# Optimization experiments

Measured on AMD Instinct MI355X. Metric: run time of the kernel, lower is better.

## Reference

```python
import jax, jax.numpy as jnp
import numpy as np

B = 1024      # molecules (segments)
K = 16        # conformers per molecule
N = B * K     # total nodes
C = 128       # in_out_dimension
HID = 256     # hidden_dimension of gate MLP
HEADS = 2
LAYERS = 2


def _leaky(x, slope):
    return jnp.where(x >= 0, x, slope * x)


def setup_inputs() -> dict:
    key = jax.random.key(0)
    ks = jax.random.split(key, 12)
    # segment ids: K conformers per molecule, sorted
    batch = jnp.repeat(jnp.arange(B, dtype=jnp.int64), K)
    # fully connected within each segment, no self loops, then append self loops
    idx = np.arange(N, dtype=np.int64).reshape(B, K)
    src = np.broadcast_to(idx[:, :, None], (B, K, K)).reshape(-1)
    dst = np.broadcast_to(idx[:, None, :], (B, K, K)).reshape(-1)
    keep = src != dst
    e_src = jnp.asarray(np.concatenate([src[keep], np.arange(N, dtype=np.int64)]))
    e_dst = jnp.asarray(np.concatenate([dst[keep], np.arange(N, dtype=np.int64)]))
    sc = 1.0 / np.sqrt(C)
    sh = 1.0 / np.sqrt(HID)
    inp = {
        "H": jax.random.normal(ks[0], (N, C), jnp.float32),
        "batch": batch,
        "edge_src": e_src,
        "edge_dst": e_dst,
        "Wl": jax.random.normal(ks[1], (LAYERS, C, HEADS * C), jnp.float32) * sc,
        "bl": jnp.zeros((LAYERS, HEADS * C), jnp.float32),
        "Wr": jax.random.normal(ks[2], (LAYERS, C, HEADS * C), jnp.float32) * sc,
        "br": jnp.zeros((LAYERS, HEADS * C), jnp.float32),
        "att": jax.random.normal(ks[3], (LAYERS, HEADS, C), jnp.float32) * sc,
        "gat_bias": jnp.zeros((LAYERS, C), jnp.float32),
        "gW1": jax.random.normal(ks[4], (C, HID), jnp.float32) * sc,
        "gb1": jnp.zeros((HID,), jnp.float32),
        "gW2": jax.random.normal(ks[5], (HID, HID), jnp.float32) * sh,
        "gb2": jnp.zeros((HID,), jnp.float32),
        "gW3": jax.random.normal(ks[6], (HID, 1), jnp.float32) * sh,
        "gb3": jnp.zeros((1,), jnp.float32),
    }
    return inp


def _segment_softmax(logits, seg, num_segments):
    m = jax.ops.segment_max(logits, seg, num_segments=num_segments)
    ex = jnp.exp(logits - m[seg])
    den = jax.ops.segment_sum(ex, seg, num_segments=num_segments)
    return ex / den[seg]


def _gatv2(x, e_src, e_dst, Wl, bl, Wr, br, att, bias):
    # GATv2Conv, concat=False (mean over heads), negative_slope=0.2
    xl = (x @ Wl + bl).reshape(N, HEADS, C)   # source transform
    xr = (x @ Wr + br).reshape(N, HEADS, C)   # target transform
    e = _leaky(xl[e_src] + xr[e_dst], 0.2)    # [E, H, C]
    logits = jnp.einsum('ehc,hc->eh', e, att) # [E, H]
    alpha = _segment_softmax(logits, e_dst, N)
    out = jax.ops.segment_sum(xl[e_src] * alpha[:, :, None], e_dst, num_segments=N)
    return out.mean(axis=1) + bias            # [N, C]


def reference(H, batch, edge_src, edge_dst, Wl, bl, Wr, br, att, gat_bias,
              gW1, gb1, gW2, gb2, gW3, gb3):
    x = H
    for l in range(LAYERS):
        x = _gatv2(x, edge_src, edge_dst, Wl[l], bl[l], Wr[l], br[l], att[l], gat_bias[l])
    # gate MLP (LeakyReLU default slope 0.01)
    h = _leaky(x @ gW1 + gb1, 0.01)
    h = _leaky(h @ gW2 + gb2, 0.01)
    h_gate = h @ gW3 + gb3                    # [N, 1]
    scores = _segment_softmax(h_gate, batch, B)
    h_pool = jax.ops.segment_sum(x * scores, batch, num_segments=B)  # [B, C]
    return (h_pool, scores)
```

## Files before the change

### kernel.cpp

```cpp
#include <hip/hip_runtime.h>
#include <hip/hip_bf16.h>
#include <math.h>

#define N_NODES 16384
#define B_MOL   1024

typedef __attribute__((ext_vector_type(8))) short short8v;
typedef __attribute__((ext_vector_type(4))) float f32x4;

static __device__ __forceinline__ unsigned short f2bf(float f) {
    unsigned int u = __float_as_uint(f);
    unsigned int r = (u + 0x7FFFu + ((u >> 16) & 1u)) >> 16;
    return (unsigned short)r;
}
static __device__ __forceinline__ float bf2f(unsigned short h) {
    return __uint_as_float(((unsigned int)h) << 16);
}

__global__ __launch_bounds__(256)
void conv_pack(const float* __restrict__ Wl, const float* __restrict__ Wr,
               const float* __restrict__ g1, const float* __restrict__ g2,
               unsigned short* __restrict__ wpk) {
    int idx = blockIdx.x * 256 + threadIdx.x;
    if (idx >= 229376) return;
    float v; size_t base; int nK, k, col;
    if (idx < 131072) {
        int l = idx >> 16;
        int e = idx & 65535;
        k = e >> 9; col = e & 511;
        v = (col < 256) ? Wl[l * 32768 + k * 256 + col]
                        : Wr[l * 32768 + k * 256 + (col - 256)];
        base = (size_t)l * 131072; nK = 4;
    } else if (idx < 163840) {
        int e = idx - 131072; k = e >> 8; col = e & 255;
        v = g1[k * 256 + col]; base = 262144; nK = 4;
    } else {
        int e = idx - 163840; k = e >> 8; col = e & 255;
        v = g2[k * 256 + col]; base = 327680; nK = 8;
    }
    int cb = col >> 4, ci = col & 15, ks = k >> 5, kk = k & 31;
    int lane = ((kk >> 3) << 4) | ci;
    size_t fo = ((size_t)(cb * nK + ks) * 2) * 512 + lane * 8 + (kk & 7);
    unsigned short h = f2bf(v);
    wpk[base + fo] = h;
    wpk[base + fo + 512] = f2bf(v - bf2f(h));
}

template<int NK, int NCB>
static __device__ __forceinline__ void tile_gemm32(
        const short* __restrict__ Ah, const short* __restrict__ Al,
        const unsigned short* __restrict__ wv,
        f32x4 (&acc)[2][NCB], int lane) {
    int lr = lane & 15;
    int kq = (lane >> 4) * 8;
    short8v bc[NCB][2], bn[NCB][2];
    #pragma unroll
    for (int j = 0; j < NCB; ++j) {
        bc[j][0] = *(const short8v*)&wv[((j * NK + 0) * 2 + 0) * 512 + lane * 8];
        bc[j][1] = *(const short8v*)&wv[((j * NK + 0) * 2 + 1) * 512 + lane * 8];
    }
    #pragma unroll
    for (int ks = 0; ks < NK; ++ks) {
        if (ks + 1 < NK) {
            #pragma unroll
            for (int j = 0; j < NCB; ++j) {
                bn[j][0] = *(const short8v*)&wv[((j * NK + ks + 1) * 2 + 0) * 512 + lane * 8];
                bn[j][1] = *(const short8v*)&wv[((j * NK + ks + 1) * 2 + 1) * 512 + lane * 8];
            }
        }
        short8v ah[2], al[2];
        #pragma unroll
        for (int i = 0; i < 2; ++i) {
            int ro = (i * 16 + lr) * 264 + ks * 32 + kq;
            ah[i] = *(const short8v*)&Ah[ro];
            al[i] = *(const short8v*)&Al[ro];
        }
        #pragma unroll
        for (int i = 0; i < 2; ++i)
            #pragma unroll
            for (int j = 0; j < NCB; ++j) {
                acc[i][j] = __builtin_amdgcn_mfma_f32_16x16x32_bf16(ah[i], bc[j][0], acc[i][j], 0, 0, 0);
                acc[i][j] = __builtin_amdgcn_mfma_f32_16x16x32_bf16(ah[i], bc[j][1], acc[i][j], 0, 0, 0);
                acc[i][j] = __builtin_amdgcn_mfma_f32_16x16x32_bf16(al[i], bc[j][0], acc[i][j], 0, 0, 0);
            }
        if (ks + 1 < NK) {
            #pragma unroll
            for (int j = 0; j < NCB; ++j) { bc[j][0] = bn[j][0]; bc[j][1] = bn[j][1]; }
        }
    }
}

static __device__ __forceinline__ void pack_pair(f32x4 o, short4* ph, short4* pl) {
    unsigned short h0 = f2bf(o[0]), h1 = f2bf(o[1]), h2 = f2bf(o[2]), h3 = f2bf(o[3]);
    *ph = make_short4((short)h0, (short)h1, (short)h2, (short)h3);
    *pl = make_short4((short)f2bf(o[0] - bf2f(h0)), (short)f2bf(o[1] - bf2f(h1)),
                      (short)f2bf(o[2] - bf2f(h2)), (short)f2bf(o[3] - bf2f(h3)));
}

__global__ __launch_bounds__(1024)
void mega(const float* __restrict__ H, const unsigned short* __restrict__ wpk,
          const float* __restrict__ bl, const float* __restrict__ br,
          const float* __restrict__ att, const float* __restrict__ gbias,
          const float* __restrict__ gb1, const float* __restrict__ gb2,
          const float* __restrict__ gW3, const float* __restrict__ gb3,
          float* __restrict__ out) {
    __shared__ short sAh[32][264], sAl[32][264];
    __shared__ float sL[32][260], sR[32][260];
    __shared__ float sLog[2][32][20];
    __shared__ float sAtt[512];
    __shared__ float sg[32], ssc[32];

    int tid  = threadIdx.x;
    int lane = tid & 63;
    int w    = tid >> 6;
    int lr   = lane & 15;
    int rowBase = blockIdx.x * 32;

    {
        int r = tid >> 5, q = tid & 31;
        f32x4 v = *(const f32x4*)&H[(size_t)(rowBase + r) * 128 + q * 4];
        pack_pair(v, (short4*)&sAh[r][q * 4], (short4*)&sAl[r][q * 4]);
        if (tid < 512) sAtt[tid] = att[tid];
    }
    __syncthreads();

    for (int l = 0; l < 2; ++l) {
        {
            #pragma unroll
            for (int p = 0; p < 2; ++p) {
                f32x4 acc[2][1];
                acc[0][0] = (f32x4){0.f, 0.f, 0.f, 0.f};
                acc[1][0] = (f32x4){0.f, 0.f, 0.f, 0.f};
                tile_gemm32<4, 1>(&sAh[0][0], &sAl[0][0],
                                  wpk + (size_t)l * 131072 + ((size_t)w * 2 + p) * 4096,
                                  acc, lane);
                float* dst; int cbase; const float* bp;
                if (w < 8) { dst = &sL[0][0]; cbase = w * 32; bp = bl + l * 256; }
                else       { dst = &sR[0][0]; cbase = (w - 8) * 32; bp = br + l * 256; }
                int cl = cbase + p * 16 + lr;
                float bv = bp[cl];
                #pragma unroll
                for (int i = 0; i < 2; ++i) {
                    int row0 = i * 16 + (lane >> 4) * 4;
                    #pragma unroll
                    for (int t = 0; t < 4; ++t)
                        dst[(row0 + t) * 260 + cl] = acc[i][0][t] + bv;
                }
            }
        }
        __syncthreads();

        {
            int m2l = tid >> 9;
            int rem = tid & 511;
            int dh  = rem >> 4;
            int s   = rem & 15;
            int d   = dh >> 1, hh = dh & 1;
            const float* xrp = &sR[m2l * 16 + d][hh * 128];
            const float* xlp = &sL[m2l * 16 + s][hh * 128];
            const float* ap  = &sAtt[l * 256 + hh * 128];
            float ac = 0.f;
            #pragma unroll 8
            for (int c4 = 0; c4 < 32; ++c4) {
                f32x4 av = *(const f32x4*)&ap[c4 * 4];
                f32x4 xv = *(const f32x4*)&xlp[c4 * 4];
                f32x4 rv = *(const f32x4*)&xrp[c4 * 4];
                f32x4 e = xv + rv;
                ac += 0.6f * av[0] * e[0] + 0.4f * av[0] * fabsf(e[0])
                    + 0.6f * av[1] * e[1] + 0.4f * av[1] * fabsf(e[1])
                    + 0.6f * av[2] * e[2] + 0.4f * av[2] * fabsf(e[2])
                    + 0.6f * av[3] * e[3] + 0.4f * av[3] * fabsf(e[3]);
            }
            float mx = ac;
            #pragma unroll
            for (int off = 1; off < 16; off <<= 1)
                mx = fmaxf(mx, __shfl_xor(mx, off, 16));
            float e = expf(ac - mx);
            float den = e;
            #pragma unroll
            for (int off = 1; off < 16; off <<= 1)
                den += __shfl_xor(den, off, 16);
            sLog[m2l][dh][s] = e / den;
        }
        __syncthreads();

        {
            int m2a = tid >> 9;
            int rem = tid & 511;
            int d  = rem >> 5;
            int cw = rem & 31;
            f32x4 f0 = (f32x4){0.f, 0.f, 0.f, 0.f};
            #pragma unroll
            for (int hh = 0; hh < 2; ++hh) {
                const float* alr = &sLog[m2a][d * 2 + hh][0];
                #pragma unroll
                for (int s = 0; s < 16; ++s) {
                    int se = (s + 2 * cw) & 15;
                    f0 += alr[se] * *(const f32x4*)&sL[m2a * 16 + se][hh * 128 + cw * 4];
                }
            }
            f32x4 o = f0 * 0.5f + *(const f32x4*)&gbias[l * 128 + cw * 4];
            int row = m2a * 16 + d;
            pack_pair(o, (short4*)&sAh[row][cw * 4], (short4*)&sAl[row][cw * 4]);
            if (l == 1)
                *(f32x4*)&sR[row][128 + cw * 4] = o;
        }
        __syncthreads();
    }

    {
        f32x4 acc[2][1];
        acc[0][0] = (f32x4){0.f, 0.f, 0.f, 0.f};
        acc[1][0] = (f32x4){0.f, 0.f, 0.f, 0.f};
        tile_gemm32<4, 1>(&sAh[0][0], &sAl[0][0],
                          wpk + 262144 + (size_t)w * 4096, acc, lane);
        __syncthreads();
        int cl = w * 16 + lr;
        float bv = gb1[cl];
        #pragma unroll
        for (int i = 0; i < 2; ++i) {
            int row0 = i * 16 + (lane >> 4) * 4;
            #pragma unroll
            for (int t = 0; t < 4; ++t) {
                float v = acc[i][0][t] + bv;
                v = v >= 0.f ? v : 0.01f * v;
                unsigned short h = f2bf(v);
                sAh[row0 + t][cl] = (short)h;
                sAl[row0 + t][cl] = (short)f2bf(v - bf2f(h));
            }
        }
    }
    __syncthreads();

    {
        f32x4 acc[2][1];
        acc[0][0] = (f32x4){0.f, 0.f, 0.f, 0.f};
        acc[1][0] = (f32x4){0.f, 0.f, 0.f, 0.f};
        tile_gemm32<8, 1>(&sAh[0][0], &sAl[0][0],
                          wpk + 327680 + (size_t)w * 8192, acc, lane);
        int cl = w * 16 + lr;
        float bv = gb2[cl];
        #pragma unroll
        for (int i = 0; i < 2; ++i) {
            int row0 = i * 16 + (lane >> 4) * 4;
            #pragma unroll
            for (int t = 0; t < 4; ++t) {
                float v = acc[i][0][t] + bv;
                v = v >= 0.f ? v : 0.01f * v;
                sL[row0 + t][cl] = v;
            }
        }
    }
    __syncthreads();

    {
        int grow = tid >> 5, l32 = tid & 31;
        f32x4 h2a = *(const f32x4*)&sL[grow][l32 * 8];
        f32x4 h2b = *(const f32x4*)&sL[grow][l32 * 8 + 4];
        f32x4 w3a = *(const f32x4*)&gW3[l32 * 8];
        f32x4 w3b = *(const f32x4*)&gW3[l32 * 8 + 4];
        float p = h2a[0] * w3a[0] + h2a[1] * w3a[1] + h2a[2] * w3a[2] + h2a[3] * w3a[3]
                + h2b[0] * w3b[0] + h2b[1] * w3b[1] + h2b[2] * w3b[2] + h2b[3] * w3b[3];
        #pragma unroll
        for (int off = 16; off; off >>= 1) p += __shfl_down(p, off, 32);
        if (l32 == 0) sg[grow] = p + gb3[0];
    }
    __syncthreads();

    if (tid < 32) {
        float v = sg[tid];
        float mx = v;
        #pragma unroll
        for (int off = 8; off; off >>= 1) mx = fmaxf(mx, __shfl_xor(mx, off, 16));
        float e = expf(v - mx);
        float den = e;
        #pragma unroll
        for (int off = 8; off; off >>= 1) den += __shfl_xor(den, off, 16);
        float sc = e / den;
        ssc[tid] = sc;
        out[131072 + rowBase + tid] = sc;
    }
    __syncthreads();

    if (tid < 256) {
        int cc = tid & 127;
        int mp = tid >> 7;
        float a = 0.f;
        #pragma unroll
        for (int s = 0; s < 16; ++s)
            a += ssc[mp * 16 + s] * sR[mp * 16 + s][128 + cc];
        out[(size_t)(blockIdx.x * 2 + mp) * 128 + cc] = a;
    }
}

extern "C" void kernel_launch(void* const* d_in, const int* in_sizes, int n_in,
                              void* d_out, int out_size, void* d_ws, size_t ws_size,
                              hipStream_t stream) {
    (void)in_sizes; (void)n_in; (void)out_size; (void)ws_size;
    const float* H        = (const float*)d_in[0];
    const float* Wl       = (const float*)d_in[4];
    const float* bl       = (const float*)d_in[5];
    const float* Wr       = (const float*)d_in[6];
    const float* br       = (const float*)d_in[7];
    const float* att      = (const float*)d_in[8];
    const float* gat_bias = (const float*)d_in[9];
    const float* gW1      = (const float*)d_in[10];
    const float* gb1      = (const float*)d_in[11];
    const float* gW2      = (const float*)d_in[12];
    const float* gb2      = (const float*)d_in[13];
    const float* gW3      = (const float*)d_in[14];
    const float* gb3      = (const float*)d_in[15];
    float* out = (float*)d_out;

    unsigned short* wpk = (unsigned short*)d_ws;

    conv_pack<<<896, 256, 0, stream>>>(Wl, Wr, gW1, gW2, wpk);
    mega<<<B_MOL / 2, 1024, 0, stream>>>(H, wpk, bl, br, att, gat_bias,
                                         gb1, gb2, gW3, gb3, out);
}
```

Measured before the change: 78.20 us.

## Process one molecule per 512-thread block instead of two per 1024-thread block

```diff
diff --git a/kernel.cpp b/kernel.cpp
--- a/kernel.cpp
+++ b/kernel.cpp
@@ -47,10 +47,10 @@
 }
 
 template<int NK, int NCB>
-static __device__ __forceinline__ void tile_gemm32(
+static __device__ __forceinline__ void tile_gemm16(
         const short* __restrict__ Ah, const short* __restrict__ Al,
         const unsigned short* __restrict__ wv,
-        f32x4 (&acc)[2][NCB], int lane) {
+        f32x4 (&acc)[NCB], int lane) {
     int lr = lane & 15;
     int kq = (lane >> 4) * 8;
     short8v bc[NCB][2], bn[NCB][2];
@@ -68,21 +68,18 @@
                 bn[j][1] = *(const short8v*)&wv[((j * NK + ks + 1) * 2 + 1) * 512 + lane * 8];
             }
         }
-        short8v ah[2], al[2];
-        #pragma unroll
-        for (int i = 0; i < 2; ++i) {
-            int ro = (i * 16 + lr) * 264 + ks * 32 + kq;
-            ah[i] = *(const short8v*)&Ah[ro];
-            al[i] = *(const short8v*)&Al[ro];
-        }
-        #pragma unroll
-        for (int i = 0; i < 2; ++i)
-            #pragma unroll
-            for (int j = 0; j < NCB; ++j) {
-                acc[i][j] = __builtin_amdgcn_mfma_f32_16x16x32_bf16(ah[i], bc[j][0], acc[i][j], 0, 0, 0);
-                acc[i][j] = __builtin_amdgcn_mfma_f32_16x16x32_bf16(ah[i], bc[j][1], acc[i][j], 0, 0, 0);
-                acc[i][j] = __builtin_amdgcn_mfma_f32_16x16x32_bf16(al[i], bc[j][0], acc[i][j], 0, 0, 0);
-            }
+        int ro = lr * 264 + ks * 32 + kq;
+        short8v ah = *(const short8v*)&Ah[ro];
+        short8v al = *(const short8v*)&Al[ro];
+        #pragma unroll
+        for (int j = 0; j < NCB; ++j)
+            acc[j] = __builtin_amdgcn_mfma_f32_16x16x32_bf16(ah, bc[j][0], acc[j], 0, 0, 0);
+        #pragma unroll
+        for (int j = 0; j < NCB; ++j)
+            acc[j] = __builtin_amdgcn_mfma_f32_16x16x32_bf16(ah, bc[j][1], acc[j], 0, 0, 0);
+        #pragma unroll
+        for (int j = 0; j < NCB; ++j)
+            acc[j] = __builtin_amdgcn_mfma_f32_16x16x32_bf16(al, bc[j][0], acc[j], 0, 0, 0);
         if (ks + 1 < NK) {
             #pragma unroll
             for (int j = 0; j < NCB; ++j) { bc[j][0] = bn[j][0]; bc[j][1] = bn[j][1]; }
@@ -97,30 +94,31 @@
                       (short)f2bf(o[2] - bf2f(h2)), (short)f2bf(o[3] - bf2f(h3)));
 }
 
-__global__ __launch_bounds__(1024)
+__global__ __launch_bounds__(512, 4)
 void mega(const float* __restrict__ H, const unsigned short* __restrict__ wpk,
           const float* __restrict__ bl, const float* __restrict__ br,
           const float* __restrict__ att, const float* __restrict__ gbias,
           const float* __restrict__ gb1, const float* __restrict__ gb2,
           const float* __restrict__ gW3, const float* __restrict__ gb3,
           float* __restrict__ out) {
-    __shared__ short sAh[32][264], sAl[32][264];
-    __shared__ float sL[32][260], sR[32][260];
-    __shared__ float sLog[2][32][20];
+    __shared__ short sAh[16][264], sAl[16][264];
+    __shared__ float sL[16][260], sR[16][260];
+    __shared__ float sLog[32][20];
     __shared__ float sAtt[512];
-    __shared__ float sg[32], ssc[32];
+    __shared__ float sg[16], ssc[16];
 
     int tid  = threadIdx.x;
     int lane = tid & 63;
     int w    = tid >> 6;
     int lr   = lane & 15;
-    int rowBase = blockIdx.x * 32;
+    int mol  = blockIdx.x;
+    int rowBase = mol * 16;
 
     {
         int r = tid >> 5, q = tid & 31;
         f32x4 v = *(const f32x4*)&H[(size_t)(rowBase + r) * 128 + q * 4];
         pack_pair(v, (short4*)&sAh[r][q * 4], (short4*)&sAl[r][q * 4]);
-        if (tid < 512) sAtt[tid] = att[tid];
+        sAtt[tid] = att[tid];
     }
     __syncthreads();
 
@@ -128,36 +126,35 @@
         {
             #pragma unroll
             for (int p = 0; p < 2; ++p) {
-                f32x4 acc[2][1];
-                acc[0][0] = (f32x4){0.f, 0.f, 0.f, 0.f};
-                acc[1][0] = (f32x4){0.f, 0.f, 0.f, 0.f};
-                tile_gemm32<4, 1>(&sAh[0][0], &sAl[0][0],
-                                  wpk + (size_t)l * 131072 + ((size_t)w * 2 + p) * 4096,
+                f32x4 acc[2];
+                acc[0] = (f32x4){0.f, 0.f, 0.f, 0.f};
+                acc[1] = (f32x4){0.f, 0.f, 0.f, 0.f};
+                int cb0 = w * 4 + p * 2;
+                tile_gemm16<4, 2>(&sAh[0][0], &sAl[0][0],
+                                  wpk + (size_t)l * 131072 + (size_t)cb0 * 4096,
                                   acc, lane);
                 float* dst; int cbase; const float* bp;
-                if (w < 8) { dst = &sL[0][0]; cbase = w * 32; bp = bl + l * 256; }
-                else       { dst = &sR[0][0]; cbase = (w - 8) * 32; bp = br + l * 256; }
-                int cl = cbase + p * 16 + lr;
-                float bv = bp[cl];
+                if (w < 4) { dst = &sL[0][0]; cbase = w * 64 + p * 32; bp = bl + l * 256; }
+                else       { dst = &sR[0][0]; cbase = (w - 4) * 64 + p * 32; bp = br + l * 256; }
+                int row0 = (lane >> 4) * 4;
                 #pragma unroll
-                for (int i = 0; i < 2; ++i) {
-                    int row0 = i * 16 + (lane >> 4) * 4;
+                for (int j = 0; j < 2; ++j) {
+                    int cl = cbase + j * 16 + lr;
+                    float bv = bp[cl];
                     #pragma unroll
                     for (int t = 0; t < 4; ++t)
-                        dst[(row0 + t) * 260 + cl] = acc[i][0][t] + bv;
+                        dst[(row0 + t) * 260 + cl] = acc[j][t] + bv;
                 }
             }
         }
         __syncthreads();
 
         {
-            int m2l = tid >> 9;
-            int rem = tid & 511;
-            int dh  = rem >> 4;
-            int s   = rem & 15;
+            int dh  = tid >> 4;
+            int s   = tid & 15;
             int d   = dh >> 1, hh = dh & 1;
-            const float* xrp = &sR[m2l * 16 + d][hh * 128];
-            const float* xlp = &sL[m2l * 16 + s][hh * 128];
+            const float* xrp = &sR[d][hh * 128];
+            const float* xlp = &sL[s][hh * 128];
             const float* ap  = &sAtt[l * 256 + hh * 128];
             float ac = 0.f;
             #pragma unroll 8
@@ -180,49 +177,46 @@
             #pragma unroll
             for (int off = 1; off < 16; off <<= 1)
                 den += __shfl_xor(den, off, 16);
-            sLog[m2l][dh][s] = e / den;
+            sLog[dh][s] = e / den;
         }
         __syncthreads();
 
         {
-            int m2a = tid >> 9;
-            int rem = tid & 511;
-            int d  = rem >> 5;
-            int cw = rem & 31;
+            int d  = tid >> 5;
+            int cw = tid & 31;
             f32x4 f0 = (f32x4){0.f, 0.f, 0.f, 0.f};
             #pragma unroll
             for (int hh = 0; hh < 2; ++hh) {
-                const float* alr = &sLog[m2a][d * 2 + hh][0];
+                const float* alr = &sLog[d * 2 + hh][0];
                 #pragma unroll
                 for (int s = 0; s < 16; ++s) {
                     int se = (s + 2 * cw) & 15;
-                    f0 += alr[se] * *(const f32x4*)&sL[m2a * 16 + se][hh * 128 + cw * 4];
+                    f0 += alr[se] * *(const f32x4*)&sL[se][hh * 128 + cw * 4];
                 }
             }
             f32x4 o = f0 * 0.5f + *(const f32x4*)&gbias[l * 128 + cw * 4];
-            int row = m2a * 16 + d;
-            pack_pair(o, (short4*)&sAh[row][cw * 4], (short4*)&sAl[row][cw * 4]);
+            pack_pair(o, (short4*)&sAh[d][cw * 4], (short4*)&sAl[d][cw * 4]);
             if (l == 1)
-                *(f32x4*)&sR[row][128 + cw * 4] = o;
+                *(f32x4*)&sR[d][128 + cw * 4] = o;
         }
         __syncthreads();
     }
 
     {
-        f32x4 acc[2][1];
-        acc[0][0] = (f32x4){0.f, 0.f, 0.f, 0.f};
-        acc[1][0] = (f32x4){0.f, 0.f, 0.f, 0.f};
-        tile_gemm32<4, 1>(&sAh[0][0], &sAl[0][0],
-                          wpk + 262144 + (size_t)w * 4096, acc, lane);
+        f32x4 acc[2];
+        acc[0] = (f32x4){0.f, 0.f, 0.f, 0.f};
+        acc[1] = (f32x4){0.f, 0.f, 0.f, 0.f};
+        tile_gemm16<4, 2>(&sAh[0][0], &sAl[0][0],
+                          wpk + 262144 + (size_t)w * 8192, acc, lane);
         __syncthreads();
-        int cl = w * 16 + lr;
-        float bv = gb1[cl];
-        #pragma unroll
-        for (int i = 0; i < 2; ++i) {
-            int row0 = i * 16 + (lane >> 4) * 4;
+        int row0 = (lane >> 4) * 4;
+        #pragma unroll
+        for (int j = 0; j < 2; ++j) {
+            int cl = w * 32 + j * 16 + lr;
+            float bv = gb1[cl];
             #pragma unroll
             for (int t = 0; t < 4; ++t) {
-                float v = acc[i][0][t] + bv;
+                float v = acc[j][t] + bv;
                 v = v >= 0.f ? v : 0.01f * v;
                 unsigned short h = f2bf(v);
                 sAh[row0 + t][cl] = (short)h;
@@ -233,19 +227,19 @@
     __syncthreads();
 
     {
-        f32x4 acc[2][1];
-        acc[0][0] = (f32x4){0.f, 0.f, 0.f, 0.f};
-        acc[1][0] = (f32x4){0.f, 0.f, 0.f, 0.f};
-        tile_gemm32<8, 1>(&sAh[0][0], &sAl[0][0],
-                          wpk + 327680 + (size_t)w * 8192, acc, lane);
-        int cl = w * 16 + lr;
-        float bv = gb2[cl];
-        #pragma unroll
-        for (int i = 0; i < 2; ++i) {
-            int row0 = i * 16 + (lane >> 4) * 4;
+        f32x4 acc[2];
+        acc[0] = (f32x4){0.f, 0.f, 0.f, 0.f};
+        acc[1] = (f32x4){0.f, 0.f, 0.f, 0.f};
+        tile_gemm16<8, 2>(&sAh[0][0], &sAl[0][0],
+                          wpk + 327680 + (size_t)w * 16384, acc, lane);
+        int row0 = (lane >> 4) * 4;
+        #pragma unroll
+        for (int j = 0; j < 2; ++j) {
+            int cl = w * 32 + j * 16 + lr;
+            float bv = gb2[cl];
             #pragma unroll
             for (int t = 0; t < 4; ++t) {
-                float v = acc[i][0][t] + bv;
+                float v = acc[j][t] + bv;
                 v = v >= 0.f ? v : 0.01f * v;
                 sL[row0 + t][cl] = v;
             }
@@ -267,7 +261,7 @@
     }
     __syncthreads();
 
-    if (tid < 32) {
+    if (tid < 16) {
         float v = sg[tid];
         float mx = v;
         #pragma unroll
@@ -282,14 +276,12 @@
     }
     __syncthreads();
 
-    if (tid < 256) {
-        int cc = tid & 127;
-        int mp = tid >> 7;
+    if (tid < 128) {
         float a = 0.f;
         #pragma unroll
         for (int s = 0; s < 16; ++s)
-            a += ssc[mp * 16 + s] * sR[mp * 16 + s][128 + cc];
-        out[(size_t)(blockIdx.x * 2 + mp) * 128 + cc] = a;
+            a += ssc[s] * sR[s][128 + tid];
+        out[(size_t)mol * 128 + tid] = a;
     }
 }
 
@@ -315,6 +307,6 @@
     unsigned short* wpk = (unsigned short*)d_ws;
 
     conv_pack<<<896, 256, 0, stream>>>(Wl, Wr, gW1, gW2, wpk);
-    mega<<<B_MOL / 2, 1024, 0, stream>>>(H, wpk, bl, br, att, gat_bias,
-                                         gb1, gb2, gW3, gb3, out);
-}
+    mega<<<B_MOL, 512, 0, stream>>>(H, wpk, bl, br, att, gat_bias,
+                                    gb1, gb2, gW3, gb3, out);
+}
```

New measurement: 82.15 us. 5.1% more time.
